# Kernel tuning notes

Measured on AMD Instinct MI355X. Metric: run time of the kernel, lower is better.

## Reference

```python
import jax, jax.numpy as jnp
import numpy as np

NEG_BIG = -9e15
ALPHA = 0.2  # LeakyReLU negative slope


def setup_inputs() -> dict:
    key = jax.random.key(0)
    k1, k2, k3, k4 = jax.random.split(key, 4)
    N, F_in, F_out = 8192, 256, 64
    inp = jax.random.normal(k1, (N, F_in), dtype=jnp.float32)
    adj = jax.random.randint(k2, (N, N), 0, 2, dtype=jnp.int32)
    W = jax.random.normal(k3, (F_in, F_out), dtype=jnp.float32) * 0.05
    a = jax.random.normal(k4, (2 * F_out, 1), dtype=jnp.float32) * 0.05
    return {"input": inp, "adj": adj, "W": W, "a": a}


def reference(input, adj, W, a):
    # h = X W : [N, F_out]
    h = input @ W
    F_out = W.shape[1]
    # a_input[i,j] = concat(h_i, h_j); a_input @ a = h@a1 broadcast over j + h@a2 broadcast over i.
    a1 = a[:F_out, 0]   # [F_out]
    a2 = a[F_out:, 0]   # [F_out]
    s1 = h @ a1         # [N]
    s2 = h @ a2         # [N]
    e = jax.nn.leaky_relu(s1[:, None] + s2[None, :], negative_slope=ALPHA)  # [N, N]
    att = jnp.where(adj > 0, e, jnp.float32(NEG_BIG))
    att = jax.nn.softmax(att, axis=1)
    # dropout is identity in eval mode (training=False)
    h_prime = att @ h   # [N, F_out]
    return jax.nn.elu(h_prime)
```

## Files before the change

kernel.cpp:

```cpp
#include <hip/hip_runtime.h>
#include <hip/hip_bf16.h>

typedef __bf16 bf16_t;
typedef __attribute__((ext_vector_type(8))) __bf16 bf16x8;
typedef __attribute__((ext_vector_type(4))) __bf16 bf16x4;
typedef __attribute__((ext_vector_type(4))) float floatx4;
typedef __attribute__((ext_vector_type(4))) int intx4;

#define NN 8192
#define FIN 256
#define FOUT 64
#define GAT_ALPHA 0.2f

__global__ __launch_bounds__(256) void gat_h_kernel(
    const float* __restrict__ input,
    const float* __restrict__ W,
    const float* __restrict__ a,
    bf16_t* __restrict__ hT,
    float* __restrict__ s1g, float* __restrict__ e1g, float* __restrict__ f1g,
    float* __restrict__ s2g, float* __restrict__ e2g, float* __restrict__ f2g)
{
    alignas(16) __shared__ bf16_t in_lds[32][264];
    alignas(16) __shared__ bf16_t wt_lds[64][264];
    __shared__ float h_lds[32][65];

    const int t  = threadIdx.x;
    const int i0 = blockIdx.x * 32;

    #pragma unroll
    for (int v = 0; v < 8; v++) {
        int u  = v * 256 + t;
        int i  = u >> 6;
        int k4 = (u & 63) * 4;
        floatx4 x = *(const floatx4*)(input + (size_t)(i0 + i) * FIN + k4);
        bf16x4 b;
        #pragma unroll
        for (int e = 0; e < 4; e++) b[e] = (bf16_t)x[e];
        *(bf16x4*)(&in_lds[i][k4]) = b;
    }
    #pragma unroll
    for (int v = 0; v < 16; v++) {
        int u  = v * 256 + t;
        int k  = u >> 4;
        int f4 = (u & 15) * 4;
        floatx4 wv = *(const floatx4*)(W + k * FOUT + f4);
        #pragma unroll
        for (int e = 0; e < 4; e++) wt_lds[f4 + e][k] = (bf16_t)wv[e];
    }
    __syncthreads();

    const int wave = t >> 6;
    const int lane = t & 63;
    const int i16  = (wave & 1) * 16;
    const int f32  = (wave >> 1) * 32;
    const int lm   = lane & 15;
    const int lq   = lane >> 4;

    floatx4 acc0 = {0.f, 0.f, 0.f, 0.f};
    floatx4 acc1 = {0.f, 0.f, 0.f, 0.f};
    #pragma unroll
    for (int ks = 0; ks < 8; ks++) {
        int ko = ks * 32 + lq * 8;
        bf16x8 af = *(const bf16x8*)(&in_lds[i16 + lm][ko]);
        bf16x8 b0 = *(const bf16x8*)(&wt_lds[f32 + lm][ko]);
        bf16x8 b1 = *(const bf16x8*)(&wt_lds[f32 + 16 + lm][ko]);
        acc0 = __builtin_amdgcn_mfma_f32_16x16x32_bf16(af, b0, acc0, 0, 0, 0);
        acc1 = __builtin_amdgcn_mfma_f32_16x16x32_bf16(af, b1, acc1, 0, 0, 0);
    }

    #pragma unroll
    for (int c = 0; c < 2; c++) {
        floatx4 acc = c ? acc1 : acc0;
        int f  = f32 + c * 16 + lm;
        int ib = i0 + i16 + lq * 4;
        bf16x4 hp;
        #pragma unroll
        for (int r = 0; r < 4; r++) hp[r] = (bf16_t)acc[r];
        *(bf16x4*)(hT + (size_t)f * NN + ib) = hp;
    }
    #pragma unroll
    for (int c = 0; c < 2; c++) {
        floatx4 acc = c ? acc1 : acc0;
        #pragma unroll
        for (int r = 0; r < 4; r++)
            h_lds[i16 + lq * 4 + r][f32 + c * 16 + lm] = acc[r];
    }
    __syncthreads();

    if (t < 64) {
        int r   = t & 31;
        int sel = t >> 5;
        const float* av = a + sel * FOUT;
        float s = 0.f;
        #pragma unroll 8
        for (int f = 0; f < FOUT; f++) s += h_lds[r][f] * av[f];
        int gi = i0 + r;
        float E = expf(s);
        float F = expf(GAT_ALPHA * s);
        if (sel == 0) { s1g[gi] = s; e1g[gi] = E; f1g[gi] = F; }
        else          { s2g[gi] = s; e2g[gi] = E; f2g[gi] = F; }
    }
}

#define LOAD_CHUNK(J0, ADJV, HV, S2V, E2V, F2V)                                \
    {                                                                          \
        S2V = *(const floatx4*)(s2g + (J0) + 4 * tj);                          \
        E2V = *(const floatx4*)(e2g + (J0) + 4 * tj);                          \
        F2V = *(const floatx4*)(f2g + (J0) + 4 * tj);                          \
        _Pragma("unroll")                                                      \
        for (int it = 0; it < 8; it++)                                         \
            ADJV[it] = *(const intx4*)(adj +                                   \
                (size_t)(i0 + it * 4 + ti) * NN + (J0) + 4 * tj);              \
        _Pragma("unroll")                                                      \
        for (int u = 0; u < 8; u++) {                                          \
            int f  = (u * 256 + t) >> 5;                                       \
            int j8 = ((u * 256 + t) & 31) * 8;                                 \
            HV[u] = *(const bf16x8*)(hT + (size_t)f * NN + (J0) + j8);         \
        }                                                                      \
    }

#define CONSUME_CHUNK(ADJV, HV, S2V, E2V, F2V)                                 \
    {                                                                          \
        _Pragma("unroll")                                                      \
        for (int it = 0; it < 8; it++) {                                       \
            int r = it * 4 + ti;                                               \
            float s1r = s1_l[r], E1 = e1_l[r], F1 = f1_l[r];                   \
            bf16x4 wq;                                                         \
            float sum = 0.f;                                                   \
            _Pragma("unroll")                                                  \
            for (int e = 0; e < 4; e++) {                                      \
                bool pos = (s1r + S2V[e]) > 0.f;                               \
                float wv = (ADJV[it][e] > 0)                                   \
                               ? (pos ? E1 * E2V[e] : F1 * F2V[e]) : 0.f;      \
                bf16_t wb = (bf16_t)wv;                                        \
                wq[e] = wb;                                                    \
                sum += (float)wb;                                              \
            }                                                                  \
            rowsum[it] += sum;                                                 \
            *(bf16x4*)(&w_lds[r][4 * tj]) = wq;                                \
        }                                                                      \
        _Pragma("unroll")                                                      \
        for (int u = 0; u < 8; u++) {                                          \
            int f  = (u * 256 + t) >> 5;                                       \
            int j8 = ((u * 256 + t) & 31) * 8;                                 \
            *(bf16x8*)(&ht_lds[f][j8]) = HV[u];                                \
        }                                                                      \
    }

#define MFMA_CHUNK()                                                           \
    {                                                                          \
        _Pragma("unroll")                                                      \
        for (int ks = 0; ks < 8; ks++) {                                       \
            int ko = ks * 32 + lq * 8;                                         \
            bf16x8 af = *(const bf16x8*)(&w_lds[i16 + lm][ko]);                \
            bf16x8 b0 = *(const bf16x8*)(&ht_lds[f32 + lm][ko]);               \
            bf16x8 b1 = *(const bf16x8*)(&ht_lds[f32 + 16 + lm][ko]);          \
            acc0 = __builtin_amdgcn_mfma_f32_16x16x32_bf16(af, b0, acc0,0,0,0);\
            acc1 = __builtin_amdgcn_mfma_f32_16x16x32_bf16(af, b1, acc1,0,0,0);\
        }                                                                      \
    }

__global__ __launch_bounds__(256) void gat_att_kernel(
    const int* __restrict__ adj,
    const bf16_t* __restrict__ hT,
    const float* __restrict__ s1g, const float* __restrict__ e1g,
    const float* __restrict__ f1g,
    const float* __restrict__ s2g, const float* __restrict__ e2g,
    const float* __restrict__ f2g,
    float* __restrict__ out)
{
    alignas(16) __shared__ bf16_t w_lds[32][264];
    alignas(16) __shared__ bf16_t ht_lds[64][264];
    __shared__ float part[32][66];
    __shared__ float s1_l[32], e1_l[32], f1_l[32];
    __shared__ float rowinv[32];

    const int t  = threadIdx.x;
    const int i0 = blockIdx.x * 32;
    const int tj = t & 63;
    const int ti = t >> 6;

    if (t < 32) {
        s1_l[t] = s1g[i0 + t];
        e1_l[t] = e1g[i0 + t];
        f1_l[t] = f1g[i0 + t];
    }
    __syncthreads();

    const int wave = t >> 6;
    const int lane = t & 63;
    const int i16  = (wave & 1) * 16;
    const int f32  = (wave >> 1) * 32;
    const int lm   = lane & 15;
    const int lq   = lane >> 4;

    floatx4 acc0 = {0.f, 0.f, 0.f, 0.f};
    floatx4 acc1 = {0.f, 0.f, 0.f, 0.f};
    float rowsum[8];
    #pragma unroll
    for (int r = 0; r < 8; r++) rowsum[r] = 0.f;

    intx4  adjA[8], adjB[8];
    bf16x8 hvA[8], hvB[8];
    floatx4 s2A, e2A, f2A, s2B, e2B, f2B;

    LOAD_CHUNK(0, adjA, hvA, s2A, e2A, f2A);

    for (int j0 = 0; j0 < NN; j0 += 512) {
        __syncthreads();
        CONSUME_CHUNK(adjA, hvA, s2A, e2A, f2A);
        LOAD_CHUNK(j0 + 256, adjB, hvB, s2B, e2B, f2B);
        __syncthreads();
        MFMA_CHUNK();

        __syncthreads();
        CONSUME_CHUNK(adjB, hvB, s2B, e2B, f2B);
        if (j0 + 512 < NN) LOAD_CHUNK(j0 + 512, adjA, hvA, s2A, e2A, f2A);
        __syncthreads();
        MFMA_CHUNK();
    }

    #pragma unroll
    for (int it = 0; it < 8; it++) part[it * 4 + ti][tj] = rowsum[it];
    __syncthreads();
    if (t < 32) {
        float s = 0.f;
        #pragma unroll 8
        for (int k = 0; k < 64; k++) s += part[t][k];
        rowinv[t] = (s > 0.f) ? 1.0f / s : 0.f;
    }
    __syncthreads();

    #pragma unroll
    for (int c = 0; c < 2; c++) {
        floatx4 acc = c ? acc1 : acc0;
        int f = f32 + c * 16 + lm;
        #pragma unroll
        for (int r = 0; r < 4; r++) {
            int i = i16 + lq * 4 + r;
            float x = acc[r] * rowinv[i];
            float y = (x > 0.f) ? x : (expf(x) - 1.0f);
            out[(size_t)(i0 + i) * FOUT + f] = y;
        }
    }
}

extern "C" void kernel_launch(void* const* d_in, const int* in_sizes, int n_in,
                              void* d_out, int out_size, void* d_ws, size_t ws_size,
                              hipStream_t stream) {
    const float* input = (const float*)d_in[0];
    const int*   adj   = (const int*)d_in[1];
    const float* W     = (const float*)d_in[2];
    const float* a     = (const float*)d_in[3];
    float*       out   = (float*)d_out;

    char* ws = (char*)d_ws;
    bf16_t* hT  = (bf16_t*)ws;
    float*  s1g = (float*)(ws + (1 << 20));
    float*  e1g = s1g + NN;
    float*  f1g = e1g + NN;
    float*  s2g = f1g + NN;
    float*  e2g = s2g + NN;
    float*  f2g = e2g + NN;

    gat_h_kernel<<<NN / 32, 256, 0, stream>>>(input, W, a, hT,
                                              s1g, e1g, f1g, s2g, e2g, f2g);
    gat_att_kernel<<<NN / 32, 256, 0, stream>>>(adj, hT,
                                                s1g, e1g, f1g, s2g, e2g, f2g,
                                                out);
}
```

Before: 405.0 us.

## Split attention kernel over two column halves with separate combine kernel

The attention kernel's j-range is split into two halves across a second grid dimension. Each half writes partial numerators and row sums to workspace, and a new combine kernel sums them, normalizes, and applies ELU. The aim is to double the block count and raise occupancy on the GPU. The cost is an extra launch and extra global traffic for the partial buffers.

```diff
diff --git a/kernel.cpp b/kernel.cpp
--- a/kernel.cpp
+++ b/kernel.cpp
@@ -11,6 +11,7 @@
 #define FIN 256
 #define FOUT 64
 #define GAT_ALPHA 0.2f
+#define JHALF (NN / 2)
 
 __global__ __launch_bounds__(256) void gat_h_kernel(
     const float* __restrict__ input,
@@ -160,25 +161,27 @@
         }                                                                      \
     }
 
-__global__ __launch_bounds__(256) void gat_att_kernel(
+__global__ __launch_bounds__(256, 2) void gat_att_kernel(
     const int* __restrict__ adj,
     const bf16_t* __restrict__ hT,
     const float* __restrict__ s1g, const float* __restrict__ e1g,
     const float* __restrict__ f1g,
     const float* __restrict__ s2g, const float* __restrict__ e2g,
     const float* __restrict__ f2g,
-    float* __restrict__ out)
+    float* __restrict__ pacc,
+    float* __restrict__ prs)
 {
     alignas(16) __shared__ bf16_t w_lds[32][264];
     alignas(16) __shared__ bf16_t ht_lds[64][264];
     __shared__ float part[32][66];
     __shared__ float s1_l[32], e1_l[32], f1_l[32];
-    __shared__ float rowinv[32];
-
-    const int t  = threadIdx.x;
-    const int i0 = blockIdx.x * 32;
-    const int tj = t & 63;
-    const int ti = t >> 6;
+
+    const int t     = threadIdx.x;
+    const int i0    = blockIdx.x * 32;
+    const int half  = blockIdx.y;
+    const int jbase = half * JHALF;
+    const int tj    = t & 63;
+    const int ti    = t >> 6;
 
     if (t < 32) {
         s1_l[t] = s1g[i0 + t];
@@ -204,9 +207,9 @@
     bf16x8 hvA[8], hvB[8];
     floatx4 s2A, e2A, f2A, s2B, e2B, f2B;
 
-    LOAD_CHUNK(0, adjA, hvA, s2A, e2A, f2A);
-
-    for (int j0 = 0; j0 < NN; j0 += 512) {
+    LOAD_CHUNK(jbase, adjA, hvA, s2A, e2A, f2A);
+
+    for (int j0 = jbase; j0 < jbase + JHALF; j0 += 512) {
         __syncthreads();
         CONSUME_CHUNK(adjA, hvA, s2A, e2A, f2A);
         LOAD_CHUNK(j0 + 256, adjB, hvB, s2B, e2B, f2B);
@@ -215,7 +218,8 @@
 
         __syncthreads();
         CONSUME_CHUNK(adjB, hvB, s2B, e2B, f2B);
-        if (j0 + 512 < NN) LOAD_CHUNK(j0 + 512, adjA, hvA, s2A, e2A, f2A);
+        if (j0 + 512 < jbase + JHALF)
+            LOAD_CHUNK(j0 + 512, adjA, hvA, s2A, e2A, f2A);
         __syncthreads();
         MFMA_CHUNK();
     }
@@ -227,10 +231,10 @@
         float s = 0.f;
         #pragma unroll 8
         for (int k = 0; k < 64; k++) s += part[t][k];
-        rowinv[t] = (s > 0.f) ? 1.0f / s : 0.f;
-    }
-    __syncthreads();
-
+        prs[half * NN + i0 + t] = s;
+    }
+
+    float* pa = pacc + (size_t)half * NN * FOUT;
     #pragma unroll
     for (int c = 0; c < 2; c++) {
         floatx4 acc = c ? acc1 : acc0;
@@ -238,11 +242,29 @@
         #pragma unroll
         for (int r = 0; r < 4; r++) {
             int i = i16 + lq * 4 + r;
-            float x = acc[r] * rowinv[i];
-            float y = (x > 0.f) ? x : (expf(x) - 1.0f);
-            out[(size_t)(i0 + i) * FOUT + f] = y;
+            pa[(size_t)(i0 + i) * FOUT + f] = acc[r];
         }
     }
+}
+
+__global__ __launch_bounds__(256) void gat_combine_kernel(
+    const float* __restrict__ pacc,
+    const float* __restrict__ prs,
+    float* __restrict__ out)
+{
+    int idx = blockIdx.x * 256 + threadIdx.x;
+    int i   = idx >> 4;
+    floatx4 a0 = *(const floatx4*)(pacc + (size_t)idx * 4);
+    floatx4 a1 = *(const floatx4*)(pacc + (size_t)NN * FOUT + (size_t)idx * 4);
+    float rs   = prs[i] + prs[NN + i];
+    float rinv = (rs > 0.f) ? 1.0f / rs : 0.f;
+    floatx4 r;
+    #pragma unroll
+    for (int e = 0; e < 4; e++) {
+        float x = (a0[e] + a1[e]) * rinv;
+        r[e] = (x > 0.f) ? x : (expf(x) - 1.0f);
+    }
+    *(floatx4*)(out + (size_t)idx * 4) = r;
 }
 
 extern "C" void kernel_launch(void* const* d_in, const int* in_sizes, int n_in,
@@ -262,10 +284,14 @@
     float*  s2g = f1g + NN;
     float*  e2g = s2g + NN;
     float*  f2g = e2g + NN;
+    float*  pacc = f2g + NN;
+    float*  prs  = pacc + 2 * NN * FOUT;
 
     gat_h_kernel<<<NN / 32, 256, 0, stream>>>(input, W, a, hT,
                                               s1g, e1g, f1g, s2g, e2g, f2g);
-    gat_att_kernel<<<NN / 32, 256, 0, stream>>>(adj, hT,
-                                                s1g, e1g, f1g, s2g, e2g, f2g,
-                                                out);
-}
+    dim3 gridB(NN / 32, 2);
+    gat_att_kernel<<<gridB, 256, 0, stream>>>(adj, hT,
+                                              s1g, e1g, f1g, s2g, e2g, f2g,
+                                              pacc, prs);
+    gat_combine_kernel<<<NN * FOUT / 4 / 256, 256, 0, stream>>>(pacc, prs, out);
+}
```

After: 583.4 us. 1.44x slower.
